# Optimization experiments

Hardware: AMD Instinct MI355X
Metric: run time of the kernel (lower is better)

The kernel has to match this reference:

```python
import jax, jax.numpy as jnp
import numpy as np


def setup_inputs() -> dict:
    key = jax.random.key(0)
    ks = jax.random.split(key, 6)
    B, S, D, E = 4, 2048, 1024, 8
    H = 4 * D
    return {
        "x": jax.random.normal(ks[0], (B, S, D), dtype=jnp.float32),
        "logits": jax.random.normal(ks[1], (B, S, E), dtype=jnp.float32),
        "noise": jax.random.normal(ks[2], (B, S, E), dtype=jnp.float32),
        "W1": jax.random.normal(ks[3], (E, D, H), dtype=jnp.float32) * (1.0 / np.sqrt(D)),
        "b1": jnp.zeros((E, H), dtype=jnp.float32),
        "W2": jax.random.normal(ks[4], (E, H, D), dtype=jnp.float32) * (1.0 / np.sqrt(H)),
        "b2": jnp.zeros((E, D), dtype=jnp.float32),
        "top_k": 2,
    }


def reference(x, logits, noise, W1, b1, W2, b2, top_k):
    # NoisyTopkRouter_Cluster: noise scaled by softplus(logits), then sparse top-k softmax
    B, S, D = x.shape
    E = logits.shape[-1]
    noisy = logits + noise * jax.nn.softplus(logits)           # [B,S,E]
    _, topi = jax.lax.top_k(noisy, top_k)                      # [B,S,K]
    in_topk = jax.nn.one_hot(topi, E, dtype=jnp.bool_).any(-2)  # [B,S,E]
    sparse = jnp.where(in_topk, noisy, -jnp.inf)
    gates = jax.nn.softmax(sparse, axis=-1)                    # [B,S,E]; zero off top-k

    # SparseMoE combine: sum_e gate[:, e] * Expert_e(x). Gate is exactly 0 for
    # unselected experts, so dense-masked compute matches the gather/scatter loop.
    xf = x.reshape(-1, D)                                      # [T,D]
    gf = gates.reshape(-1, E).T                                # [E,T]

    def body(acc, params):
        w1, bb1, w2, bb2, g = params                           # g: [T]
        h = jax.nn.relu(xf @ w1 + bb1)                         # [T,4D]
        acc = acc + (h @ w2 + bb2) * g[:, None]
        return acc, None

    acc, _ = jax.lax.scan(body, jnp.zeros_like(xf), (W1, b1, W2, b2, gf))
    return acc.reshape(B, S, D)
```

## Files before the change

kernel.cpp:

```cpp
#include <hip/hip_runtime.h>
#include <cstdint>
#include <cstddef>

#define T_TOK 8192
#define E_NUM 8
#define D_DIM 1024
#define H_DIM 4096
#define MAXTILES 72
#define TILE 256

typedef __attribute__((ext_vector_type(8))) short short8;
typedef __attribute__((ext_vector_type(4))) float f32x4;
typedef __attribute__((ext_vector_type(8))) unsigned short ushort8v;
typedef __attribute__((ext_vector_type(4))) unsigned short ushort4v;

__device__ __forceinline__ unsigned short f2b(float f) {
  unsigned int u = __float_as_uint(f);
  u += 0x7fffu + ((u >> 16) & 1u);
  return (unsigned short)(u >> 16);
}

__device__ __forceinline__ void async16(const void* g, void* l) {
  __builtin_amdgcn_global_load_lds((const __attribute__((address_space(1))) void*)g,
                                   (__attribute__((address_space(3))) void*)l, 16, 0, 0);
}

__global__ void router_kernel(const float* __restrict__ logits, const float* __restrict__ noise,
                              int* __restrict__ counts, int* __restrict__ ti, float* __restrict__ tg) {
  int tk = blockIdx.x * blockDim.x + threadIdx.x;
  if (tk >= T_TOK) return;
  float nz[E_NUM];
#pragma unroll
  for (int e = 0; e < E_NUM; ++e) {
    float l = logits[tk * E_NUM + e];
    float sp = fmaxf(l, 0.f) + log1pf(expf(-fabsf(l)));
    nz[e] = l + noise[tk * E_NUM + e] * sp;
  }
  int i1 = 0; float v1 = nz[0];
#pragma unroll
  for (int e = 1; e < E_NUM; ++e) if (nz[e] > v1) { v1 = nz[e]; i1 = e; }
  int i2 = -1; float v2 = -3.0e38f;
#pragma unroll
  for (int e = 0; e < E_NUM; ++e) if (e != i1 && nz[e] > v2) { v2 = nz[e]; i2 = e; }
  float ex = expf(v2 - v1);
  float g1 = 1.f / (1.f + ex);
  float g2 = ex / (1.f + ex);
  int s1 = atomicAdd(&counts[i1], 1);
  int s2 = atomicAdd(&counts[i2], 1);
  ti[tk*4+0] = i1; ti[tk*4+1] = s1; ti[tk*4+2] = i2; ti[tk*4+3] = s2;
  tg[tk*2+0] = g1; tg[tk*2+1] = g2;
}

__global__ void setup_kernel(const int* __restrict__ counts, int* __restrict__ offs,
                             int* __restrict__ tab) {
  int o = 0;
  for (int e = 0; e < E_NUM; ++e) { offs[e] = o; o += counts[e]; }
  offs[E_NUM] = o;
  int mt = 0;
  for (int e = 0; e < E_NUM; ++e)
    for (int m0 = 0; m0 < counts[e]; m0 += TILE) { tab[mt*2] = e; tab[mt*2+1] = m0; ++mt; }
  for (; mt < MAXTILES; ++mt) { tab[mt*2] = -1; tab[mt*2+1] = 0; }
}

__global__ void gather_kernel(const float* __restrict__ x, const int* __restrict__ ti,
                              const float* __restrict__ tg, const int* __restrict__ offs,
                              unsigned short* __restrict__ xg, int* __restrict__ stok,
                              float* __restrict__ sg) {
  const int tk = blockIdx.x, t = threadIdx.x;
  const int i1 = ti[tk*4+0], s1 = ti[tk*4+1], i2 = ti[tk*4+2], s2 = ti[tk*4+3];
  const int r1 = offs[i1] + s1, r2 = offs[i2] + s2;
  if (t == 0) {
    stok[r1] = tk; sg[r1] = tg[tk*2+0];
    stok[r2] = tk; sg[r2] = tg[tk*2+1];
  }
  const float4 v = *(const float4*)(x + (size_t)tk * D_DIM + t * 4);
  ushort4v bb; bb.x = f2b(v.x); bb.y = f2b(v.y); bb.z = f2b(v.z); bb.w = f2b(v.w);
  *(ushort4v*)(xg + (size_t)r1 * D_DIM + t * 4) = bb;
  *(ushort4v*)(xg + (size_t)r2 * D_DIM + t * 4) = bb;
}

__global__ void transpose_kernel(const float* __restrict__ W, unsigned short* __restrict__ Wt,
                                 int K, int N) {
  const int e = blockIdx.z;
  const float* We = W + (size_t)e * K * N;
  unsigned short* Wte = Wt + (size_t)e * K * N;
  __shared__ __align__(16) unsigned short tb[64 * 72];
  const int n0 = blockIdx.x * 64, k0 = blockIdx.y * 64;
  const int t = threadIdx.x;
  const int kr = t >> 4;
  const int c4 = (t & 15) * 4;
#pragma unroll
  for (int rr = 0; rr < 4; ++rr) {
    int k = kr + rr * 16;
    const float4 v = *(const float4*)(We + (size_t)(k0 + k) * N + n0 + c4);
    tb[(c4+0)*72 + k] = f2b(v.x);
    tb[(c4+1)*72 + k] = f2b(v.y);
    tb[(c4+2)*72 + k] = f2b(v.z);
    tb[(c4+3)*72 + k] = f2b(v.w);
  }
  __syncthreads();
  const int n = t >> 2, kq = (t & 3) * 16;
  ushort8v a = *(const ushort8v*)&tb[n*72 + kq];
  ushort8v b = *(const ushort8v*)&tb[n*72 + kq + 8];
  *(ushort8v*)(Wte + (size_t)(n0+n)*K + k0 + kq) = a;
  *(ushort8v*)(Wte + (size_t)(n0+n)*K + k0 + kq + 8) = b;
}

template<int EPI, int NX, int KSPLIT>
__global__ __launch_bounds__(512, 2)
void gemm8p(const unsigned short* __restrict__ A, const unsigned short* __restrict__ Bt,
            const int K, const int N,
            const int* __restrict__ counts, const int* __restrict__ offs,
            const int* __restrict__ tab,
            const float* __restrict__ bias,
            unsigned short* __restrict__ Hout,
            float* __restrict__ Out,
            const int* __restrict__ slot_tok, const float* __restrict__ slot_gate) {
  constexpr int GRID = NX * MAXTILES * KSPLIT;
  constexpr int Q = GRID / 8;
  const int bid = blockIdx.x;
  const int lin = (bid & 7) * Q + (bid >> 3);
  const int mt  = lin % MAXTILES;
  const int u   = lin / MAXTILES;
  const int kb  = u % KSPLIT;
  const int xi  = u / KSPLIT;

  const int e = tab[mt*2];
  if (e < 0) return;
  const int m0  = tab[mt*2+1];
  const int cnt = counts[e];
  const int seg = offs[e];
  const int n0  = xi * TILE;
  const int KC  = K / KSPLIT;
  const int NT  = KC / 64;
  const int ks  = kb * KC;

  __shared__ __align__(16) short smem[2 * 32768];
  __shared__ int   s_tok[TILE];
  __shared__ float s_g[TILE];

  const int t = threadIdx.x;
  const int lane = t & 63;
  const int wv = t >> 6;
  const int wm = wv >> 2, wn = wv & 3;
  const int fr = lane & 15, fq = lane >> 4;

  if (EPI == 1 && t < TILE) {
    int rl = m0 + t;
    if (rl < cnt) { s_tok[t] = slot_tok[seg + rl]; s_g[t] = slot_gate[seg + rl]; }
    else          { s_tok[t] = 0;                  s_g[t] = 0.f; }
  }
  __syncthreads();

  const unsigned short* Ae = A + (size_t)seg * K;
  const unsigned short* Be = Bt + (size_t)e * N * K + (size_t)n0 * K;

  const int rl   = wv * 8 + (lane >> 3);
  const int swSt = ((lane & 7) ^ (lane >> 3)) * 8;
  int am0 = m0 + rl;        am0 = am0 < cnt ? am0 : cnt - 1;
  int am1 = m0 + rl + 64;   am1 = am1 < cnt ? am1 : cnt - 1;
  int am2 = m0 + rl + 128;  am2 = am2 < cnt ? am2 : cnt - 1;
  int am3 = m0 + rl + 192;  am3 = am3 < cnt ? am3 : cnt - 1;
  const unsigned short* pa0 = Ae + (size_t)am0 * K + swSt;
  const unsigned short* pa1 = Ae + (size_t)am1 * K + swSt;
  const unsigned short* pa2 = Ae + (size_t)am2 * K + swSt;
  const unsigned short* pa3 = Ae + (size_t)am3 * K + swSt;
  const unsigned short* pb0 = Be + (size_t)(rl)       * K + swSt;
  const unsigned short* pb1 = Be + (size_t)(rl + 64)  * K + swSt;
  const unsigned short* pb2 = Be + (size_t)(rl + 128) * K + swSt;
  const unsigned short* pb3 = Be + (size_t)(rl + 192) * K + swSt;
  const int wvOff = wv * 1024;

  auto issueA0 = [&](int par, int ko) {
    char* d = (char*)smem + par * 65536 + wvOff;
    async16(pa0 + ko, d); async16(pa1 + ko, d + 8192);
  };
  auto issueA1 = [&](int par, int ko) {
    char* d = (char*)smem + par * 65536 + 16384 + wvOff;
    async16(pa2 + ko, d); async16(pa3 + ko, d + 8192);
  };
  auto issueB0 = [&](int par, int ko) {
    char* d = (char*)smem + par * 65536 + 32768 + wvOff;
    async16(pb0 + ko, d); async16(pb1 + ko, d + 8192);
  };
  auto issueB1 = [&](int par, int ko) {
    char* d = (char*)smem + par * 65536 + 49152 + wvOff;
    async16(pb2 + ko, d); async16(pb3 + ko, d + 8192);
  };

  const int sw0 = ((0 * 4 + fq) ^ (fr & 7)) * 8;
  const int sw1 = ((1 * 4 + fq) ^ (fr & 7)) * 8;
  const int bl  = (wn & 1) * 64;

  f32x4 acc[8][4];
#pragma unroll
  for (int i = 0; i < 8; ++i)
#pragma unroll
    for (int j = 0; j < 4; ++j) acc[i][j] = (f32x4){0.f, 0.f, 0.f, 0.f};

  issueB0(0, ks); issueB1(0, ks);
  issueA0(0, ks); issueA1(0, ks);
  issueB0(1, ks + 64); issueB1(1, ks + 64);
  asm volatile("s_waitcnt vmcnt(4)" ::: "memory");
  asm volatile("s_barrier" ::: "memory");

  short8 aLo[4][2], aHi[4][2], b01[2][2], b23[2][2];

  for (int kt = 0; kt < NT; ++kt) {
    const short* bR = smem + (kt & 1) * 32768;
    const short* Aw = bR + wm * 8192;
    const short* Bw = bR + 16384 + (wn >> 1) * 8192;
    const int parA = (kt + 1) & 1, parB = kt & 1;
    int tA = kt + 1; if (tA > NT - 1) tA = NT - 1;
    int tB = kt + 2; if (tB > NT - 1) tB = NT - 1;
    const int kA = ks + tA * 64, kB = ks + tB * 64;

#pragma unroll
    for (int i = 0; i < 4; ++i) {
      int ro = (i * 16 + fr) * 64;
      aLo[i][0] = *(const short8*)&Aw[ro + sw0];
      aLo[i][1] = *(const short8*)&Aw[ro + sw1];
    }
#pragma unroll
    for (int j = 0; j < 2; ++j) {
      int ro = (bl + j * 16 + fr) * 64;
      b01[j][0] = *(const short8*)&Bw[ro + sw0];
      b01[j][1] = *(const short8*)&Bw[ro + sw1];
    }
    issueA0(parA, kA);
    asm volatile("s_barrier" ::: "memory");
    __builtin_amdgcn_s_setprio(1);
#pragma unroll
    for (int i = 0; i < 4; ++i)
#pragma unroll
      for (int j = 0; j < 2; ++j) {
        acc[i][j] = __builtin_amdgcn_mfma_f32_16x16x32_bf16(aLo[i][0], b01[j][0], acc[i][j], 0, 0, 0);
        acc[i][j] = __builtin_amdgcn_mfma_f32_16x16x32_bf16(aLo[i][1], b01[j][1], acc[i][j], 0, 0, 0);
      }
    __builtin_amdgcn_s_setprio(0);
    asm volatile("s_barrier" ::: "memory");

#pragma unroll
    for (int j = 0; j < 2; ++j) {
      int ro = (bl + 32 + j * 16 + fr) * 64;
      b23[j][0] = *(const short8*)&Bw[ro + sw0];
      b23[j][1] = *(const short8*)&Bw[ro + sw1];
    }
    issueA1(parA, kA);
    asm volatile("s_barrier" ::: "memory");
    __builtin_amdgcn_s_setprio(1);
#pragma unroll
    for (int i = 0; i < 4; ++i)
#pragma unroll
      for (int j = 0; j < 2; ++j) {
        acc[i][j+2] = __builtin_amdgcn_mfma_f32_16x16x32_bf16(aLo[i][0], b23[j][0], acc[i][j+2], 0, 0, 0);
        acc[i][j+2] = __builtin_amdgcn_mfma_f32_16x16x32_bf16(aLo[i][1], b23[j][1], acc[i][j+2], 0, 0, 0);
      }
    __builtin_amdgcn_s_setprio(0);
    asm volatile("s_barrier" ::: "memory");

#pragma unroll
    for (int i = 0; i < 4; ++i) {
      int ro = ((i + 4) * 16 + fr) * 64;
      aHi[i][0] = *(const short8*)&Aw[ro + sw0];
      aHi[i][1] = *(const short8*)&Aw[ro + sw1];
    }
    issueB0(parB, kB);
    asm volatile("s_barrier" ::: "memory");
    __builtin_amdgcn_s_setprio(1);
#pragma unroll
    for (int i = 0; i < 4; ++i)
#pragma unroll
      for (int j = 0; j < 2; ++j) {
        acc[i+4][j+2] = __builtin_amdgcn_mfma_f32_16x16x32_bf16(aHi[i][0], b23[j][0], acc[i+4][j+2], 0, 0, 0);
        acc[i+4][j+2] = __builtin_amdgcn_mfma_f32_16x16x32_bf16(aHi[i][1], b23[j][1], acc[i+4][j+2], 0, 0, 0);
      }
    __builtin_amdgcn_s_setprio(0);
    asm volatile("s_barrier" ::: "memory");

    issueB1(parB, kB);
    asm volatile("s_barrier" ::: "memory");
    __builtin_amdgcn_s_setprio(1);
#pragma unroll
    for (int i = 0; i < 4; ++i)
#pragma unroll
      for (int j = 0; j < 2; ++j) {
        acc[i+4][j] = __builtin_amdgcn_mfma_f32_16x16x32_bf16(aHi[i][0], b01[j][0], acc[i+4][j], 0, 0, 0);
        acc[i+4][j] = __builtin_amdgcn_mfma_f32_16x16x32_bf16(aHi[i][1], b01[j][1], acc[i+4][j], 0, 0, 0);
      }
    __builtin_amdgcn_s_setprio(0);
    asm volatile("s_waitcnt vmcnt(4)" ::: "memory");
    asm volatile("s_barrier" ::: "memory");
  }

  if (EPI == 0) {
    const float* be = bias + (size_t)e * N;
#pragma unroll
    for (int j = 0; j < 4; ++j) {
      int col = n0 + wn*64 + j*16 + fr;
      float bv = be[col];
#pragma unroll
      for (int i = 0; i < 8; ++i) {
        int tl0 = wm*128 + i*16 + fq*4;
#pragma unroll
        for (int r = 0; r < 4; ++r) {
          int tlr = tl0 + r;
          if (m0 + tlr < cnt) {
            float v = acc[i][j][r] + bv;
            v = v > 0.f ? v : 0.f;
            Hout[(size_t)(seg + m0 + tlr) * N + col] = f2b(v);
          }
        }
      }
    }
  } else {
    const float* be = bias + (size_t)e * N;
#pragma unroll
    for (int j = 0; j < 4; ++j) {
      int col = n0 + wn*64 + j*16 + fr;
      float bv = (kb == 0) ? be[col] : 0.f;
#pragma unroll
      for (int i = 0; i < 8; ++i) {
        int tl0 = wm*128 + i*16 + fq*4;
#pragma unroll
        for (int r = 0; r < 4; ++r) {
          int tlr = tl0 + r;
          if (m0 + tlr < cnt) {
            float v = (acc[i][j][r] + bv) * s_g[tlr];
            unsafeAtomicAdd(Out + (size_t)s_tok[tlr] * N + col, v);
          }
        }
      }
    }
  }
}

extern "C" void kernel_launch(void* const* d_in, const int* in_sizes, int n_in,
                              void* d_out, int out_size, void* d_ws, size_t ws_size,
                              hipStream_t stream) {
  const float* x      = (const float*)d_in[0];
  const float* logits = (const float*)d_in[1];
  const float* noise  = (const float*)d_in[2];
  const float* W1     = (const float*)d_in[3];
  const float* b1     = (const float*)d_in[4];
  const float* W2     = (const float*)d_in[5];
  const float* b2     = (const float*)d_in[6];
  float* out = (float*)d_out;

  char* ws = (char*)d_ws;
  size_t off = 0;
  auto alloc = [&](size_t b) { size_t o = off; off = (off + b + 255) & ~(size_t)255; return o; };
  size_t o_counts = alloc(E_NUM * 4);
  size_t o_offs   = alloc((E_NUM + 1) * 4);
  size_t o_tab    = alloc((size_t)MAXTILES * 2 * 4);
  size_t o_ti     = alloc((size_t)T_TOK * 4 * 4);
  size_t o_tg     = alloc((size_t)T_TOK * 2 * 4);
  size_t o_stok   = alloc((size_t)2 * T_TOK * 4);
  size_t o_sg     = alloc((size_t)2 * T_TOK * 4);
  size_t o_xg     = alloc((size_t)2 * T_TOK * D_DIM * 2);
  size_t o_w1t    = alloc((size_t)E_NUM * D_DIM * H_DIM * 2);
  size_t o_w2t    = alloc((size_t)E_NUM * D_DIM * H_DIM * 2);
  size_t o_h      = alloc((size_t)2 * T_TOK * H_DIM * 2);
  if (off > ws_size) return;

  int*            counts = (int*)(ws + o_counts);
  int*            offsp  = (int*)(ws + o_offs);
  int*            tab    = (int*)(ws + o_tab);
  int*            ti     = (int*)(ws + o_ti);
  float*          tg     = (float*)(ws + o_tg);
  int*            stok   = (int*)(ws + o_stok);
  float*          sg     = (float*)(ws + o_sg);
  unsigned short* xg     = (unsigned short*)(ws + o_xg);
  unsigned short* w1t    = (unsigned short*)(ws + o_w1t);
  unsigned short* w2t    = (unsigned short*)(ws + o_w2t);
  unsigned short* h      = (unsigned short*)(ws + o_h);

  hipMemsetAsync(out, 0, (size_t)out_size * sizeof(float), stream);
  hipMemsetAsync(counts, 0, E_NUM * sizeof(int), stream);

  router_kernel<<<T_TOK / 256, 256, 0, stream>>>(logits, noise, counts, ti, tg);
  setup_kernel<<<1, 1, 0, stream>>>(counts, offsp, tab);
  gather_kernel<<<T_TOK, 256, 0, stream>>>(x, ti, tg, offsp, xg, stok, sg);

  transpose_kernel<<<dim3(H_DIM/64, D_DIM/64, E_NUM), 256, 0, stream>>>(W1, w1t, D_DIM, H_DIM);
  transpose_kernel<<<dim3(D_DIM/64, H_DIM/64, E_NUM), 256, 0, stream>>>(W2, w2t, H_DIM, D_DIM);

  gemm8p<0, H_DIM/TILE, 1><<<dim3((H_DIM/TILE) * MAXTILES * 1), 512, 0, stream>>>(
      xg, w1t, D_DIM, H_DIM, counts, offsp, tab, b1, h, nullptr, nullptr, nullptr);
  gemm8p<1, D_DIM/TILE, 2><<<dim3((D_DIM/TILE) * MAXTILES * 2), 512, 0, stream>>>(
      h, w2t, H_DIM, D_DIM, counts, offsp, tab, b2, nullptr, out, stok, sg);
}
```

Measured before the change: 972.6 us.

## Replace 8-phase interleaved GEMM pipeline with simple 2-stage double buffer

```diff
diff --git a/kernel.cpp b/kernel.cpp
--- a/kernel.cpp
+++ b/kernel.cpp
@@ -108,7 +108,7 @@
 
 template<int EPI, int NX, int KSPLIT>
 __global__ __launch_bounds__(512, 2)
-void gemm8p(const unsigned short* __restrict__ A, const unsigned short* __restrict__ Bt,
+void gemm2p(const unsigned short* __restrict__ A, const unsigned short* __restrict__ Bt,
             const int K, const int N,
             const int* __restrict__ counts, const int* __restrict__ offs,
             const int* __restrict__ tab,
@@ -171,21 +171,12 @@
   const unsigned short* pb3 = Be + (size_t)(rl + 192) * K + swSt;
   const int wvOff = wv * 1024;
 
-  auto issueA0 = [&](int par, int ko) {
+  auto stage = [&](int par, int ko) {
     char* d = (char*)smem + par * 65536 + wvOff;
-    async16(pa0 + ko, d); async16(pa1 + ko, d + 8192);
-  };
-  auto issueA1 = [&](int par, int ko) {
-    char* d = (char*)smem + par * 65536 + 16384 + wvOff;
-    async16(pa2 + ko, d); async16(pa3 + ko, d + 8192);
-  };
-  auto issueB0 = [&](int par, int ko) {
-    char* d = (char*)smem + par * 65536 + 32768 + wvOff;
-    async16(pb0 + ko, d); async16(pb1 + ko, d + 8192);
-  };
-  auto issueB1 = [&](int par, int ko) {
-    char* d = (char*)smem + par * 65536 + 49152 + wvOff;
-    async16(pb2 + ko, d); async16(pb3 + ko, d + 8192);
+    async16(pa0 + ko, d);          async16(pa1 + ko, d + 8192);
+    async16(pa2 + ko, d + 16384);  async16(pa3 + ko, d + 24576);
+    async16(pb0 + ko, d + 32768);  async16(pb1 + ko, d + 40960);
+    async16(pb2 + ko, d + 49152);  async16(pb3 + ko, d + 57344);
   };
 
   const int sw0 = ((0 * 4 + fq) ^ (fr & 7)) * 8;
@@ -198,23 +189,19 @@
 #pragma unroll
     for (int j = 0; j < 4; ++j) acc[i][j] = (f32x4){0.f, 0.f, 0.f, 0.f};
 
-  issueB0(0, ks); issueB1(0, ks);
-  issueA0(0, ks); issueA1(0, ks);
-  issueB0(1, ks + 64); issueB1(1, ks + 64);
-  asm volatile("s_waitcnt vmcnt(4)" ::: "memory");
+  stage(0, ks);
+  asm volatile("s_waitcnt vmcnt(0)" ::: "memory");
   asm volatile("s_barrier" ::: "memory");
 
   short8 aLo[4][2], aHi[4][2], b01[2][2], b23[2][2];
 
   for (int kt = 0; kt < NT; ++kt) {
-    const short* bR = smem + (kt & 1) * 32768;
+    const int cur = kt & 1;
+    if (kt + 1 < NT) stage(cur ^ 1, ks + (kt + 1) * 64);
+
+    const short* bR = smem + cur * 32768;
     const short* Aw = bR + wm * 8192;
     const short* Bw = bR + 16384 + (wn >> 1) * 8192;
-    const int parA = (kt + 1) & 1, parB = kt & 1;
-    int tA = kt + 1; if (tA > NT - 1) tA = NT - 1;
-    int tB = kt + 2; if (tB > NT - 1) tB = NT - 1;
-    const int kA = ks + tA * 64, kB = ks + tB * 64;
-
 #pragma unroll
     for (int i = 0; i < 4; ++i) {
       int ro = (i * 16 + fr) * 64;
@@ -222,74 +209,41 @@
       aLo[i][1] = *(const short8*)&Aw[ro + sw1];
     }
 #pragma unroll
+    for (int i = 0; i < 4; ++i) {
+      int ro = ((i + 4) * 16 + fr) * 64;
+      aHi[i][0] = *(const short8*)&Aw[ro + sw0];
+      aHi[i][1] = *(const short8*)&Aw[ro + sw1];
+    }
+#pragma unroll
     for (int j = 0; j < 2; ++j) {
       int ro = (bl + j * 16 + fr) * 64;
       b01[j][0] = *(const short8*)&Bw[ro + sw0];
       b01[j][1] = *(const short8*)&Bw[ro + sw1];
     }
-    issueA0(parA, kA);
-    asm volatile("s_barrier" ::: "memory");
-    __builtin_amdgcn_s_setprio(1);
-#pragma unroll
-    for (int i = 0; i < 4; ++i)
-#pragma unroll
-      for (int j = 0; j < 2; ++j) {
-        acc[i][j] = __builtin_amdgcn_mfma_f32_16x16x32_bf16(aLo[i][0], b01[j][0], acc[i][j], 0, 0, 0);
-        acc[i][j] = __builtin_amdgcn_mfma_f32_16x16x32_bf16(aLo[i][1], b01[j][1], acc[i][j], 0, 0, 0);
-      }
-    __builtin_amdgcn_s_setprio(0);
-    asm volatile("s_barrier" ::: "memory");
-
 #pragma unroll
     for (int j = 0; j < 2; ++j) {
       int ro = (bl + 32 + j * 16 + fr) * 64;
       b23[j][0] = *(const short8*)&Bw[ro + sw0];
       b23[j][1] = *(const short8*)&Bw[ro + sw1];
     }
-    issueA1(parA, kA);
-    asm volatile("s_barrier" ::: "memory");
+
     __builtin_amdgcn_s_setprio(1);
 #pragma unroll
     for (int i = 0; i < 4; ++i)
 #pragma unroll
       for (int j = 0; j < 2; ++j) {
-        acc[i][j+2] = __builtin_amdgcn_mfma_f32_16x16x32_bf16(aLo[i][0], b23[j][0], acc[i][j+2], 0, 0, 0);
-        acc[i][j+2] = __builtin_amdgcn_mfma_f32_16x16x32_bf16(aLo[i][1], b23[j][1], acc[i][j+2], 0, 0, 0);
-      }
-    __builtin_amdgcn_s_setprio(0);
-    asm volatile("s_barrier" ::: "memory");
-
-#pragma unroll
-    for (int i = 0; i < 4; ++i) {
-      int ro = ((i + 4) * 16 + fr) * 64;
-      aHi[i][0] = *(const short8*)&Aw[ro + sw0];
-      aHi[i][1] = *(const short8*)&Aw[ro + sw1];
-    }
-    issueB0(parB, kB);
-    asm volatile("s_barrier" ::: "memory");
-    __builtin_amdgcn_s_setprio(1);
-#pragma unroll
-    for (int i = 0; i < 4; ++i)
-#pragma unroll
-      for (int j = 0; j < 2; ++j) {
+        acc[i][j]     = __builtin_amdgcn_mfma_f32_16x16x32_bf16(aLo[i][0], b01[j][0], acc[i][j], 0, 0, 0);
+        acc[i][j]     = __builtin_amdgcn_mfma_f32_16x16x32_bf16(aLo[i][1], b01[j][1], acc[i][j], 0, 0, 0);
+        acc[i][j+2]   = __builtin_amdgcn_mfma_f32_16x16x32_bf16(aLo[i][0], b23[j][0], acc[i][j+2], 0, 0, 0);
+        acc[i][j+2]   = __builtin_amdgcn_mfma_f32_16x16x32_bf16(aLo[i][1], b23[j][1], acc[i][j+2], 0, 0, 0);
+        acc[i+4][j]   = __builtin_amdgcn_mfma_f32_16x16x32_bf16(aHi[i][0], b01[j][0], acc[i+4][j], 0, 0, 0);
+        acc[i+4][j]   = __builtin_amdgcn_mfma_f32_16x16x32_bf16(aHi[i][1], b01[j][1], acc[i+4][j], 0, 0, 0);
         acc[i+4][j+2] = __builtin_amdgcn_mfma_f32_16x16x32_bf16(aHi[i][0], b23[j][0], acc[i+4][j+2], 0, 0, 0);
         acc[i+4][j+2] = __builtin_amdgcn_mfma_f32_16x16x32_bf16(aHi[i][1], b23[j][1], acc[i+4][j+2], 0, 0, 0);
       }
     __builtin_amdgcn_s_setprio(0);
-    asm volatile("s_barrier" ::: "memory");
-
-    issueB1(parB, kB);
-    asm volatile("s_barrier" ::: "memory");
-    __builtin_amdgcn_s_setprio(1);
-#pragma unroll
-    for (int i = 0; i < 4; ++i)
-#pragma unroll
-      for (int j = 0; j < 2; ++j) {
-        acc[i+4][j] = __builtin_amdgcn_mfma_f32_16x16x32_bf16(aHi[i][0], b01[j][0], acc[i+4][j], 0, 0, 0);
-        acc[i+4][j] = __builtin_amdgcn_mfma_f32_16x16x32_bf16(aHi[i][1], b01[j][1], acc[i+4][j], 0, 0, 0);
-      }
-    __builtin_amdgcn_s_setprio(0);
-    asm volatile("s_waitcnt vmcnt(4)" ::: "memory");
+
+    asm volatile("s_waitcnt vmcnt(0)" ::: "memory");
     asm volatile("s_barrier" ::: "memory");
   }
 
@@ -385,8 +339,8 @@
   transpose_kernel<<<dim3(H_DIM/64, D_DIM/64, E_NUM), 256, 0, stream>>>(W1, w1t, D_DIM, H_DIM);
   transpose_kernel<<<dim3(D_DIM/64, H_DIM/64, E_NUM), 256, 0, stream>>>(W2, w2t, H_DIM, D_DIM);
 
-  gemm8p<0, H_DIM/TILE, 1><<<dim3((H_DIM/TILE) * MAXTILES * 1), 512, 0, stream>>>(
+  gemm2p<0, H_DIM/TILE, 1><<<dim3((H_DIM/TILE) * MAXTILES * 1), 512, 0, stream>>>(
       xg, w1t, D_DIM, H_DIM, counts, offsp, tab, b1, h, nullptr, nullptr, nullptr);
-  gemm8p<1, D_DIM/TILE, 2><<<dim3((D_DIM/TILE) * MAXTILES * 2), 512, 0, stream>>>(
+  gemm2p<1, D_DIM/TILE, 1><<<dim3((D_DIM/TILE) * MAXTILES * 1), 512, 0, stream>>>(
       h, w2t, H_DIM, D_DIM, counts, offsp, tab, b2, nullptr, out, stok, sg);
 }
```

After: 1.014 ms. +4.2%, slower.
